# Optimization experiments

Hardware: AMD Instinct MI355X
Metric: run time of the kernel (lower is better)

The kernel has to match this reference:

```python
import jax, jax.numpy as jnp
import numpy as np

B, N, S, C, H = 16, 64, 4096, 768, 8
HD = C // H
SCALE = HD ** -0.5
ASSIGN_EPS = 1.0


def hard_softmax(logits, axis):
    # softmax over `axis`, then straight-through one-hot argmax along `axis`
    y_soft = jax.nn.softmax(logits, axis=axis)
    idx = jnp.argmax(y_soft, axis=axis, keepdims=True)
    n = logits.shape[axis]
    shape = [1] * logits.ndim
    shape[axis] = n
    iota = jnp.arange(n).reshape(shape)
    y_hard = (iota == idx).astype(logits.dtype)
    return y_hard - jax.lax.stop_gradient(y_soft) + y_soft


def setup_inputs() -> dict:
    key = jax.random.key(0)
    ks = jax.random.split(key, 7)
    w = lambda k, shp: (jax.random.normal(k, shp, dtype=jnp.float32) * 0.02)
    return {
        'query': jax.random.normal(ks[0], (B, N, C), dtype=jnp.float32),
        'key_in': jax.random.normal(ks[1], (B, S, C), dtype=jnp.float32),
        'Wq': w(ks[2], (C, C)),
        'Wk': w(ks[3], (C, C)),
        'Wv': w(ks[4], (C, C)),
        'Wo': w(ks[5], (C, C)),
        'bo': jnp.zeros((C,), dtype=jnp.float32),
    }


def reference(query, key_in, Wq, Wk, Wv, Wo, bo):
    # linear projections (torch Linear: x @ W.T), split heads -> b h n d
    q = jnp.einsum('bnc,dc->bnd', query, Wq).reshape(B, N, H, HD).transpose(0, 2, 1, 3)
    k = jnp.einsum('bsc,dc->bsd', key_in, Wk).reshape(B, S, H, HD).transpose(0, 2, 1, 3)
    v = jnp.einsum('bsc,dc->bsd', key_in, Wv).reshape(B, S, H, HD).transpose(0, 2, 1, 3)
    raw_attn = jnp.einsum('bhnd,bhsd->bhns', q, k) * SCALE      # [B,H,N,S]
    attn = hard_softmax(raw_attn, axis=-2)                       # hard assign over groups N
    attn = attn / (attn.sum(axis=-1, keepdims=True) + ASSIGN_EPS)  # renorm over tokens S
    out = jnp.einsum('bhns,bhsd->bhnd', attn, v)                 # [B,H,N,HD]
    out = out.transpose(0, 2, 1, 3).reshape(B, N, C)
    out = jnp.einsum('bnc,dc->bnd', out, Wo) + bo
    return out
```

## Files before the change

kernel.cpp:

```cpp
#include <hip/hip_runtime.h>

#define BB 16
#define NN 64
#define SS 4096
#define CC 768
#define HH 8
#define HD 96

typedef __attribute__((ext_vector_type(8))) short bf16x8;
typedef __attribute__((ext_vector_type(4))) float f32x4;

static __device__ __forceinline__ unsigned short f2bf(float x) {
  unsigned u = __float_as_uint(x);
  unsigned r = (u + 0x7fffu + ((u >> 16) & 1u)) >> 16;
  return (unsigned short)r;
}
static __device__ __forceinline__ float bf2f(unsigned short h) {
  return __uint_as_float(((unsigned)h) << 16);
}
static __device__ __forceinline__ void split2t(float f0, float f1,
                                               unsigned* hw, unsigned* lw) {
  unsigned u0 = __float_as_uint(f0), u1 = __float_as_uint(f1);
  *hw = (u0 >> 16) | (u1 & 0xffff0000u);
  float l0 = f0 - __uint_as_float(u0 & 0xffff0000u);
  float l1 = f1 - __uint_as_float(u1 & 0xffff0000u);
  unsigned v0 = __float_as_uint(l0), v1 = __float_as_uint(l1);
  *lw = (v0 >> 16) | (v1 & 0xffff0000u);
}

__global__ __launch_bounds__(256) void k_transpose(
    const float* __restrict__ src, float* __restrict__ dst) {
  __shared__ float tile[32][33];
  const int bx = blockIdx.x % 24, by = blockIdx.x / 24;
  const int tx = threadIdx.x & 31, ty = threadIdx.x >> 5;
#pragma unroll
  for (int k = 0; k < 4; ++k)
    tile[ty + k * 8][tx] = src[(size_t)(by * 32 + ty + k * 8) * CC + bx * 32 + tx];
  __syncthreads();
#pragma unroll
  for (int k = 0; k < 4; ++k)
    dst[(size_t)(bx * 32 + ty + k * 8) * CC + by * 32 + tx] = tile[tx][ty + k * 8];
}

__global__ __launch_bounds__(256) void k_qkfold(
    const float* __restrict__ query, const float* __restrict__ WqT,
    const float* __restrict__ Wk, double* __restrict__ qk64,
    unsigned short* __restrict__ qhp, unsigned short* __restrict__ qlp) {
  __shared__ double qin[2][CC];
  __shared__ double q64[2][CC];
  const int tid = threadIdx.x;
  const int r0 = blockIdx.x * 2;

#pragma unroll
  for (int u = 0; u < 6; ++u) {
    int idx = tid + u * 256;
    int r = idx / CC, c = idx - r * CC;
    qin[r][c] = (double)query[(size_t)(r0 + r) * CC + c];
  }
  __syncthreads();

  {
    double a00 = 0.0, a01 = 0.0, a02 = 0.0;
    double a10 = 0.0, a11 = 0.0, a12 = 0.0;
    const float* wt = WqT + tid;
    for (int e = 0; e < CC; ++e) {
      const double q0 = qin[0][e], q1 = qin[1][e];
      const float* w = wt + (size_t)e * CC;
      const double w0 = (double)w[0], w1 = (double)w[256], w2 = (double)w[512];
      a00 += q0 * w0; a01 += q0 * w1; a02 += q0 * w2;
      a10 += q1 * w0; a11 += q1 * w1; a12 += q1 * w2;
    }
    q64[0][tid] = a00; q64[0][tid + 256] = a01; q64[0][tid + 512] = a02;
    q64[1][tid] = a10; q64[1][tid + 256] = a11; q64[1][tid + 512] = a12;
  }
  __syncthreads();

  const double SC = 0.10206207261596575;
  for (int h = 0; h < HH; ++h) {
    double b00 = 0.0, b01 = 0.0, b02 = 0.0;
    double b10 = 0.0, b11 = 0.0, b12 = 0.0;
    const float* wk = Wk + (size_t)(h * HD) * CC + tid;
    const double* qh0 = &q64[0][h * HD];
    const double* qh1 = &q64[1][h * HD];
#pragma unroll 4
    for (int dd = 0; dd < HD; ++dd) {
      const float* w = wk + (size_t)dd * CC;
      const double w0 = (double)w[0], w1 = (double)w[256], w2 = (double)w[512];
      const double q0 = qh0[dd], q1 = qh1[dd];
      b00 += q0 * w0; b01 += q0 * w1; b02 += q0 * w2;
      b10 += q1 * w0; b11 += q1 * w1; b12 += q1 * w2;
    }
    double av[2][3] = {{b00 * SC, b01 * SC, b02 * SC},
                       {b10 * SC, b11 * SC, b12 * SC}};
#pragma unroll
    for (int r = 0; r < 2; ++r) {
      const int row = r0 + r, b_ = row >> 6, n = row & 63;
      const int col512 = h * 64 + n;
#pragma unroll
      for (int m = 0; m < 3; ++m) {
        const int c = tid + m * 256;
        size_t o = ((size_t)(b_ * HH + h) * NN + n) * CC + c;
        qk64[o] = av[r][m];
        float f = (float)av[r][m];
        unsigned short hh16 = f2bf(f);
        const int cs = c >> 5, lkc = (c >> 3) & 3, j = c & 7;
        size_t po = (((size_t)(b_ * 24 + cs) * 32 + (col512 >> 4)) * 64 +
                     (lkc * 16 + (col512 & 15))) * 8 + j;
        qhp[po] = hh16;
        qlp[po] = f2bf(f - bf2f(hh16));
      }
    }
  }
}

#define DELTA 1e-3f

__global__ __launch_bounds__(512) void k_filter_mfma(
    const float* __restrict__ key,
    const unsigned short* __restrict__ qhp, const unsigned short* __restrict__ qlp,
    unsigned char* __restrict__ assign_t, int* __restrict__ susp,
    int* __restrict__ scnt) {
  __shared__ float alds[2][64][68];
  const int tid = threadIdx.x;
  const int lane = tid & 63;
  const int wn = tid >> 6;
  const int bid0 = blockIdx.x;
  const int swz = (bid0 & 7) * 128 + (bid0 >> 3);
  const int b = swz >> 6;
  const int s0 = (swz & 63) * 64;
  const int l16 = lane & 15;
  const int lk = lane >> 4;

  f32x4 acc[4][4];
#pragma unroll
  for (int m = 0; m < 4; ++m)
#pragma unroll
    for (int n = 0; n < 4; ++n) acc[m][n] = (f32x4){0.f, 0.f, 0.f, 0.f};

  const float* kbase = key + ((size_t)b * SS + s0) * CC;
  const int srow = tid >> 3, sc8 = tid & 7;

#define BBASE(cs) ((((size_t)(b * 24 + (cs)) * 32 + wn * 4) * 64 + lane) * 8)

  bf16x8 bhA[4], blA[4], bhB[4], blB[4];
  {
    float4 st0 = *(const float4*)(kbase + (size_t)srow * CC + sc8 * 8);
    float4 st1 = *(const float4*)(kbase + (size_t)srow * CC + sc8 * 8 + 4);
    *(float4*)&alds[0][srow][sc8 * 8] = st0;
    *(float4*)&alds[0][srow][sc8 * 8 + 4] = st1;
    const size_t bb = BBASE(0);
#pragma unroll
    for (int n = 0; n < 4; ++n) {
      bhA[n] = *(const bf16x8*)(qhp + bb + (size_t)n * 512);
      blA[n] = *(const bf16x8*)(qlp + bb + (size_t)n * 512);
    }
  }
  __syncthreads();

  for (int t = 0; t < 12; ++t) {
    const int cur = t & 1;
    float4 st0, st1;
    if (t < 11) {
      const int cb = (t + 1) * 64;
      st0 = *(const float4*)(kbase + (size_t)srow * CC + cb + sc8 * 8);
      st1 = *(const float4*)(kbase + (size_t)srow * CC + cb + sc8 * 8 + 4);
    }
    {
      const int cs = t * 2;
      const size_t bbn = BBASE(cs + 1);
#pragma unroll
      for (int n = 0; n < 4; ++n) {
        bhB[n] = *(const bf16x8*)(qhp + bbn + (size_t)n * 512);
        blB[n] = *(const bf16x8*)(qlp + bbn + (size_t)n * 512);
      }
      union { bf16x8 v; unsigned w[4]; } ah[4], al[4];
#pragma unroll
      for (int m = 0; m < 4; ++m) {
        const float* ap = &alds[cur][m * 16 + l16][lk * 8];
        float4 x0 = *(const float4*)ap;
        float4 x1 = *(const float4*)(ap + 4);
        split2t(x0.x, x0.y, &ah[m].w[0], &al[m].w[0]);
        split2t(x0.z, x0.w, &ah[m].w[1], &al[m].w[1]);
        split2t(x1.x, x1.y, &ah[m].w[2], &al[m].w[2]);
        split2t(x1.z, x1.w, &ah[m].w[3], &al[m].w[3]);
      }
#pragma unroll
      for (int m = 0; m < 4; ++m)
#pragma unroll
        for (int n = 0; n < 4; ++n)
          acc[m][n] = __builtin_amdgcn_mfma_f32_16x16x32_bf16(ah[m].v, bhA[n], acc[m][n], 0, 0, 0);
#pragma unroll
      for (int m = 0; m < 4; ++m)
#pragma unroll
        for (int n = 0; n < 4; ++n)
          acc[m][n] = __builtin_amdgcn_mfma_f32_16x16x32_bf16(ah[m].v, blA[n], acc[m][n], 0, 0, 0);
#pragma unroll
      for (int m = 0; m < 4; ++m)
#pragma unroll
        for (int n = 0; n < 4; ++n)
          acc[m][n] = __builtin_amdgcn_mfma_f32_16x16x32_bf16(al[m].v, bhA[n], acc[m][n], 0, 0, 0);
    }
    {
      if (t < 11) {
        const size_t bbn = BBASE(t * 2 + 2);
#pragma unroll
        for (int n = 0; n < 4; ++n) {
          bhA[n] = *(const bf16x8*)(qhp + bbn + (size_t)n * 512);
          blA[n] = *(const bf16x8*)(qlp + bbn + (size_t)n * 512);
        }
      }
      union { bf16x8 v; unsigned w[4]; } ah[4], al[4];
#pragma unroll
      for (int m = 0; m < 4; ++m) {
        const float* ap = &alds[cur][m * 16 + l16][32 + lk * 8];
        float4 x0 = *(const float4*)ap;
        float4 x1 = *(const float4*)(ap + 4);
        split2t(x0.x, x0.y, &ah[m].w[0], &al[m].w[0]);
        split2t(x0.z, x0.w, &ah[m].w[1], &al[m].w[1]);
        split2t(x1.x, x1.y, &ah[m].w[2], &al[m].w[2]);
        split2t(x1.z, x1.w, &ah[m].w[3], &al[m].w[3]);
      }
#pragma unroll
      for (int m = 0; m < 4; ++m)
#pragma unroll
        for (int n = 0; n < 4; ++n)
          acc[m][n] = __builtin_amdgcn_mfma_f32_16x16x32_bf16(ah[m].v, bhB[n], acc[m][n], 0, 0, 0);
#pragma unroll
      for (int m = 0; m < 4; ++m)
#pragma unroll
        for (int n = 0; n < 4; ++n)
          acc[m][n] = __builtin_amdgcn_mfma_f32_16x16x32_bf16(ah[m].v, blB[n], acc[m][n], 0, 0, 0);
#pragma unroll
      for (int m = 0; m < 4; ++m)
#pragma unroll
        for (int n = 0; n < 4; ++n)
          acc[m][n] = __builtin_amdgcn_mfma_f32_16x16x32_bf16(al[m].v, bhB[n], acc[m][n], 0, 0, 0);
    }

    if (t < 11) {
      *(float4*)&alds[cur ^ 1][srow][sc8 * 8] = st0;
      *(float4*)&alds[cur ^ 1][srow][sc8 * 8 + 4] = st1;
    }
    __syncthreads();
  }
#undef BBASE

#pragma unroll
  for (int m = 0; m < 4; ++m) {
    const int tokbase = s0 + m * 16 + lk * 4;
#pragma unroll
    for (int r = 0; r < 4; ++r) {
      const int tok = tokbase + r;
      float m1 = -3.402823466e38f, m2 = -3.402823466e38f;
      int i1 = 0;
#pragma unroll
      for (int n = 0; n < 4; ++n) {
        float v = acc[m][n][r];
        int g = n * 16 + l16;
        if (v > m1) { m2 = m1; m1 = v; i1 = g; }
        else if (v > m2) m2 = v;
      }
#pragma unroll
      for (int off = 1; off <= 8; off <<= 1) {
        float om1 = __shfl_xor(m1, off);
        float om2 = __shfl_xor(m2, off);
        int oi1 = __shfl_xor(i1, off);
        if (om1 > m1 || (om1 == m1 && oi1 < i1)) {
          m2 = fmaxf(m1, fmaxf(m2, om2));
          m1 = om1; i1 = oi1;
        } else {
          m2 = fmaxf(om1, fmaxf(m2, om2));
        }
      }
      if (l16 == 0) {
        const int bh2 = b * 8 + wn;
        assign_t[((size_t)b * SS + tok) * 8 + wn] = (unsigned char)i1;
        if (m1 - m2 < DELTA) {
          int w = atomicAdd(&scnt[bh2], 1);
          susp[(size_t)bh2 * SS + w] = tok;
        }
      }
    }
  }
}

__global__ __launch_bounds__(256) void k_rescore(
    const float* __restrict__ key, const double* __restrict__ qk64,
    const int* __restrict__ susp, const int* __restrict__ scnt,
    unsigned char* __restrict__ assign_t) {
  __shared__ float krow[16][CC];
  __shared__ double l64[16][64];
  const int bh = blockIdx.x;
  const int cnt = scnt[bh];
  if (cnt == 0) return;
  const int b = bh >> 3, h = bh & 7;
  const int tid = threadIdx.x;
  const int n = tid >> 2, q = tid & 3;
  const double* qrow = qk64 + ((size_t)bh * NN + n) * CC + q * 192;

  for (int i0 = 0; i0 < cnt; i0 += 16) {
    const int nb = (cnt - i0 < 16) ? (cnt - i0) : 16;
    for (int r = 0; r < nb; ++r) {
      const int s = susp[(size_t)bh * SS + i0 + r];
      for (int u = tid; u < CC; u += 256)
        krow[r][u] = key[((size_t)b * SS + s) * CC + u];
    }
    __syncthreads();

    double acc[16];
#pragma unroll
    for (int r = 0; r < 16; ++r) acc[r] = 0.0;
    for (int c4 = 0; c4 < 48; ++c4) {
      const double w0 = qrow[c4 * 4 + 0];
      const double w1 = qrow[c4 * 4 + 1];
      const double w2 = qrow[c4 * 4 + 2];
      const double w3 = qrow[c4 * 4 + 3];
#pragma unroll
      for (int r = 0; r < 16; ++r) {
        float4 k4 = *(const float4*)&krow[r][q * 192 + c4 * 4];
        acc[r] += w0 * (double)k4.x;
        acc[r] += w1 * (double)k4.y;
        acc[r] += w2 * (double)k4.z;
        acc[r] += w3 * (double)k4.w;
      }
    }
#pragma unroll
    for (int r = 0; r < 16; ++r) {
      acc[r] += __shfl_xor(acc[r], 1);
      acc[r] += __shfl_xor(acc[r], 2);
    }
    if (q == 0) {
#pragma unroll
      for (int r = 0; r < 16; ++r) l64[r][n] = acc[r];
    }
    __syncthreads();
    if (tid < nb) {
      double best = l64[tid][0];
      int bi = 0;
      for (int n2 = 1; n2 < 64; ++n2)
        if (l64[tid][n2] > best) { best = l64[tid][n2]; bi = n2; }
      const int s = susp[(size_t)bh * SS + i0 + tid];
      assign_t[((size_t)b * SS + s) * 8 + h] = (unsigned char)bi;
    }
    __syncthreads();
  }
}

__global__ __launch_bounds__(256) void k_counts(
    const unsigned char* __restrict__ assign_t, int* __restrict__ counts) {
  __shared__ int hist[64];
  const int bh = blockIdx.x;
  const int b = bh >> 3, h = bh & 7;
  const int tid = threadIdx.x;
  if (tid < 64) hist[tid] = 0;
  __syncthreads();
  for (int s = tid; s < SS; s += 256)
    atomicAdd(&hist[assign_t[((size_t)b * SS + s) * 8 + h]], 1);
  __syncthreads();
  if (tid < 64) counts[bh * 64 + tid] = hist[tid];
}

__global__ __launch_bounds__(64) void k_rank(
    const unsigned char* __restrict__ assign_t, const int* __restrict__ counts,
    int* __restrict__ offsets, int* __restrict__ perm) {
  __shared__ int base[64];
  const int bh = blockIdx.x;
  const int b = bh >> 3, h = bh & 7;
  const int lane = threadIdx.x;

  int cn = counts[bh * 64 + lane];
  int off = cn;
#pragma unroll
  for (int d = 1; d < 64; d <<= 1) {
    int t = __shfl_up(off, d);
    if (lane >= d) off += t;
  }
  off -= cn;
  offsets[bh * 64 + lane] = off;
  base[lane] = off;

  for (int c = 0; c < SS / 64; ++c) {
    const int s = c * 64 + lane;
    const int g = (int)assign_t[((size_t)b * SS + s) * 8 + h];
    unsigned long long m = ~0ull;
#pragma unroll
    for (int k = 0; k < 6; ++k) {
      unsigned long long bk = __ballot((g >> k) & 1);
      m &= ((g >> k) & 1) ? bk : ~bk;
    }
    const int leader = __ffsll((unsigned long long)m) - 1;
    const int rankin = __popcll(m & ((1ull << lane) - 1ull));
    int baseo = 0;
    if (lane == leader) {
      baseo = base[g];
      base[g] = baseo + __popcll(m);
    }
    baseo = __shfl(baseo, leader);
    perm[(size_t)bh * SS + baseo + rankin] = s;
  }
}

__global__ __launch_bounds__(64) void k_gatherp(
    const float* __restrict__ key, const int* __restrict__ perm,
    const int* __restrict__ offsets, const int* __restrict__ counts,
    float* __restrict__ gsum) {
  const int bid = blockIdx.x;
  const int bh = bid >> 6;
  const int b = bh >> 3;
  const int lane = threadIdx.x;

  const int off = offsets[bid];
  const int cnt = counts[bid];
  const int* pl = perm + (size_t)bh * SS + off;
  const float* kb = key + (size_t)b * SS * CC;

  float4 a0 = {0.f, 0.f, 0.f, 0.f}, b0 = a0, c0 = a0;
  int j = 0;
  for (; j + 3 < cnt; j += 4) {
    const int s0 = pl[j], s1 = pl[j + 1], s2 = pl[j + 2], s3 = pl[j + 3];
    const float4* k0 = (const float4*)(kb + (size_t)s0 * CC);
    const float4* k1 = (const float4*)(kb + (size_t)s1 * CC);
    const float4* k2 = (const float4*)(kb + (size_t)s2 * CC);
    const float4* k3 = (const float4*)(kb + (size_t)s3 * CC);
    float4 x0 = k0[lane], x1 = k0[lane + 64], x2 = k0[lane + 128];
    float4 y0 = k1[lane], y1 = k1[lane + 64], y2 = k1[lane + 128];
    float4 z0 = k2[lane], z1 = k2[lane + 64], z2 = k2[lane + 128];
    float4 w0 = k3[lane], w1 = k3[lane + 64], w2 = k3[lane + 128];
    a0.x += x0.x; a0.y += x0.y; a0.z += x0.z; a0.w += x0.w;
    b0.x += x1.x; b0.y += x1.y; b0.z += x1.z; b0.w += x1.w;
    c0.x += x2.x; c0.y += x2.y; c0.z += x2.z; c0.w += x2.w;
    a0.x += y0.x; a0.y += y0.y; a0.z += y0.z; a0.w += y0.w;
    b0.x += y1.x; b0.y += y1.y; b0.z += y1.z; b0.w += y1.w;
    c0.x += y2.x; c0.y += y2.y; c0.z += y2.z; c0.w += y2.w;
    a0.x += z0.x; a0.y += z0.y; a0.z += z0.z; a0.w += z0.w;
    b0.x += z1.x; b0.y += z1.y; b0.z += z1.z; b0.w += z1.w;
    c0.x += z2.x; c0.y += z2.y; c0.z += z2.z; c0.w += z2.w;
    a0.x += w0.x; a0.y += w0.y; a0.z += w0.z; a0.w += w0.w;
    b0.x += w1.x; b0.y += w1.y; b0.z += w1.z; b0.w += w1.w;
    c0.x += w2.x; c0.y += w2.y; c0.z += w2.z; c0.w += w2.w;
  }
  for (; j < cnt; ++j) {
    const int s0 = pl[j];
    const float4* k0 = (const float4*)(kb + (size_t)s0 * CC);
    float4 x0 = k0[lane], x1 = k0[lane + 64], x2 = k0[lane + 128];
    a0.x += x0.x; a0.y += x0.y; a0.z += x0.z; a0.w += x0.w;
    b0.x += x1.x; b0.y += x1.y; b0.z += x1.z; b0.w += x1.w;
    c0.x += x2.x; c0.y += x2.y; c0.z += x2.z; c0.w += x2.w;
  }
  float4* go = (float4*)(gsum + (size_t)bid * CC);
  go[lane] = a0; go[lane + 64] = b0; go[lane + 128] = c0;
}

__global__ __launch_bounds__(256) void k_out(
    const float* __restrict__ gsum, const int* __restrict__ counts,
    const float* __restrict__ WvT, const float* __restrict__ WoT,
    const float* __restrict__ bo, float* __restrict__ out) {
  __shared__ float gs[2][HH][CC];
  __shared__ float vr[2][CC];
  const int tid = threadIdx.x;
  const int r0 = blockIdx.x * 2;

  for (int r = 0; r < 2; ++r) {
    int row = r0 + r, b = row >> 6, n = row & 63;
    for (int h = 0; h < HH; ++h) {
      const float sc = 1.f / (float)(counts[(b * HH + h) * NN + n] + 1);
      const float* src = gsum + ((size_t)(b * HH + h) * NN + n) * CC;
      for (int m = 0; m < 3; ++m)
        gs[r][h][tid + m * 256] = src[tid + m * 256] * sc;
    }
  }
  __syncthreads();

  const int h0 = tid / HD, h1 = (tid + 256) / HD, h2 = (tid + 512) / HD;
  {
    float a00 = 0.f, a01 = 0.f, a02 = 0.f;
    float a10 = 0.f, a11 = 0.f, a12 = 0.f;
    const float* wt = WvT + tid;
    for (int e4 = 0; e4 < CC / 4; ++e4) {
      const int e = e4 * 4;
      float4 g00 = *(const float4*)&gs[0][h0][e];
      float4 g01 = *(const float4*)&gs[0][h1][e];
      float4 g02 = *(const float4*)&gs[0][h2][e];
      float4 g10 = *(const float4*)&gs[1][h0][e];
      float4 g11 = *(const float4*)&gs[1][h1][e];
      float4 g12 = *(const float4*)&gs[1][h2][e];
      const float* w0p = wt + (size_t)e * CC;
      const float* w1p = wt + (size_t)(e + 1) * CC;
      const float* w2p = wt + (size_t)(e + 2) * CC;
      const float* w3p = wt + (size_t)(e + 3) * CC;
      float wa = w0p[0], wb = w0p[256], wc = w0p[512];
      a00 = fmaf(g00.x, wa, a00); a01 = fmaf(g01.x, wb, a01); a02 = fmaf(g02.x, wc, a02);
      a10 = fmaf(g10.x, wa, a10); a11 = fmaf(g11.x, wb, a11); a12 = fmaf(g12.x, wc, a12);
      wa = w1p[0]; wb = w1p[256]; wc = w1p[512];
      a00 = fmaf(g00.y, wa, a00); a01 = fmaf(g01.y, wb, a01); a02 = fmaf(g02.y, wc, a02);
      a10 = fmaf(g10.y, wa, a10); a11 = fmaf(g11.y, wb, a11); a12 = fmaf(g12.y, wc, a12);
      wa = w2p[0]; wb = w2p[256]; wc = w2p[512];
      a00 = fmaf(g00.z, wa, a00); a01 = fmaf(g01.z, wb, a01); a02 = fmaf(g02.z, wc, a02);
      a10 = fmaf(g10.z, wa, a10); a11 = fmaf(g11.z, wb, a11); a12 = fmaf(g12.z, wc, a12);
      wa = w3p[0]; wb = w3p[256]; wc = w3p[512];
      a00 = fmaf(g00.w, wa, a00); a01 = fmaf(g01.w, wb, a01); a02 = fmaf(g02.w, wc, a02);
      a10 = fmaf(g10.w, wa, a10); a11 = fmaf(g11.w, wb, a11); a12 = fmaf(g12.w, wc, a12);
    }
    vr[0][tid] = a00; vr[0][tid + 256] = a01; vr[0][tid + 512] = a02;
    vr[1][tid] = a10; vr[1][tid + 256] = a11; vr[1][tid + 512] = a12;
  }
  __syncthreads();

  {
    float a00 = bo[tid], a01 = bo[tid + 256], a02 = bo[tid + 512];
    float a10 = a00, a11 = a01, a12 = a02;
    const float* wt = WoT + tid;
    for (int e4 = 0; e4 < CC / 4; ++e4) {
      const int e = e4 * 4;
      float4 v0 = *(const float4*)&vr[0][e];
      float4 v1 = *(const float4*)&vr[1][e];
      const float* w0p = wt + (size_t)e * CC;
      const float* w1p = wt + (size_t)(e + 1) * CC;
      const float* w2p = wt + (size_t)(e + 2) * CC;
      const float* w3p = wt + (size_t)(e + 3) * CC;
      float wa = w0p[0], wb = w0p[256], wc = w0p[512];
      a00 = fmaf(v0.x, wa, a00); a01 = fmaf(v0.x, wb, a01); a02 = fmaf(v0.x, wc, a02);
      a10 = fmaf(v1.x, wa, a10); a11 = fmaf(v1.x, wb, a11); a12 = fmaf(v1.x, wc, a12);
      wa = w1p[0]; wb = w1p[256]; wc = w1p[512];
      a00 = fmaf(v0.y, wa, a00); a01 = fmaf(v0.y, wb, a01); a02 = fmaf(v0.y, wc, a02);
      a10 = fmaf(v1.y, wa, a10); a11 = fmaf(v1.y, wb, a11); a12 = fmaf(v1.y, wc, a12);
      wa = w2p[0]; wb = w2p[256]; wc = w2p[512];
      a00 = fmaf(v0.z, wa, a00); a01 = fmaf(v0.z, wb, a01); a02 = fmaf(v0.z, wc, a02);
      a10 = fmaf(v1.z, wa, a10); a11 = fmaf(v1.z, wb, a11); a12 = fmaf(v1.z, wc, a12);
      wa = w3p[0]; wb = w3p[256]; wc = w3p[512];
      a00 = fmaf(v0.w, wa, a00); a01 = fmaf(v0.w, wb, a01); a02 = fmaf(v0.w, wc, a02);
      a10 = fmaf(v1.w, wa, a10); a11 = fmaf(v1.w, wb, a11); a12 = fmaf(v1.w, wc, a12);
    }
    out[(size_t)(r0 + 0) * CC + tid] = a00;
    out[(size_t)(r0 + 0) * CC + tid + 256] = a01;
    out[(size_t)(r0 + 0) * CC + tid + 512] = a02;
    out[(size_t)(r0 + 1) * CC + tid] = a10;
    out[(size_t)(r0 + 1) * CC + tid + 256] = a11;
    out[(size_t)(r0 + 1) * CC + tid + 512] = a12;
  }
}

extern "C" void kernel_launch(void* const* d_in, const int* in_sizes, int n_in,
                              void* d_out, int out_size, void* d_ws, size_t ws_size,
                              hipStream_t stream) {
  const float* query = (const float*)d_in[0];
  const float* key   = (const float*)d_in[1];
  const float* Wq    = (const float*)d_in[2];
  const float* Wk    = (const float*)d_in[3];
  const float* Wv    = (const float*)d_in[4];
  const float* Wo    = (const float*)d_in[5];
  const float* bo    = (const float*)d_in[6];
  float* out = (float*)d_out;

  char* ws = (char*)d_ws;
  double* qk64           = (double*)(ws);
  float* gsum            = (float*)(ws);
  unsigned short* qhp    = (unsigned short*)(ws + 50331648);
  unsigned short* qlp    = (unsigned short*)(ws + 62914560);
  unsigned char* assign_t= (unsigned char*)(ws + 75497472);
  int* susp              = (int*)(ws + 76021760);
  int* scnt              = (int*)(ws + 78118912);
  int* counts            = (int*)(ws + 78119424);
  int* offsets           = (int*)(ws + 78152192);
  int* perm              = (int*)(ws + 78184960);
  float* WqT             = (float*)(ws + 80282112);
  float* WvT             = (float*)(ws + 82641408);
  float* WoT             = (float*)(ws + 85000704);

  hipMemsetAsync(scnt, 0, 512, stream);
  k_transpose<<<576, 256, 0, stream>>>(Wq, WqT);
  k_transpose<<<576, 256, 0, stream>>>(Wv, WvT);
  k_transpose<<<576, 256, 0, stream>>>(Wo, WoT);
  k_qkfold<<<512, 256, 0, stream>>>(query, WqT, Wk, qk64, qhp, qlp);
  k_filter_mfma<<<1024, 512, 0, stream>>>(key, qhp, qlp, assign_t, susp, scnt);
  k_rescore<<<128, 256, 0, stream>>>(key, qk64, susp, scnt, assign_t);
  k_counts<<<128, 256, 0, stream>>>(assign_t, counts);
  k_rank<<<128, 64, 0, stream>>>(assign_t, counts, offsets, perm);
  k_gatherp<<<8192, 64, 0, stream>>>(key, perm, offsets, counts, gsum);
  k_out<<<512, 256, 0, stream>>>(gsum, counts, WvT, WoT, bo, out);
}
```

Measured before the change: 883.8 us.

## Pre-convert key to bf16 in half-batch chunks before gather-sum

Adds a conversion kernel that turns one half of the batch's key tensor into bf16 in workspace. The gather-sum then reads bf16 rows instead of fp32, split into two passes of eight batches each so the converted buffer stays small. The goal is to halve the bytes each head's gather pulls from memory, since every key row is read once per head. In exchange it adds an extra full read and half-size write of the key tensor, and it introduces bf16 rounding into the group sums, which could hurt accuracy against the fp32 reference.

```diff
diff --git a/kernel.cpp b/kernel.cpp
--- a/kernel.cpp
+++ b/kernel.cpp
@@ -9,6 +9,7 @@
 
 typedef __attribute__((ext_vector_type(8))) short bf16x8;
 typedef __attribute__((ext_vector_type(4))) float f32x4;
+typedef __attribute__((ext_vector_type(8))) unsigned short u16x8;
 
 static __device__ __forceinline__ unsigned short f2bf(float x) {
   unsigned u = __float_as_uint(x);
@@ -360,6 +361,21 @@
   if (tid < 64) counts[bh * 64 + tid] = hist[tid];
 }
 
+__global__ __launch_bounds__(256) void k_convert(
+    const float* __restrict__ keyhalf, unsigned short* __restrict__ kb16) {
+  const int n8 = 8 * SS * CC / 8;
+  int i = blockIdx.x * 256 + threadIdx.x;
+  const int stride = gridDim.x * 256;
+  for (; i < n8; i += stride) {
+    float4 a = ((const float4*)keyhalf)[i * 2];
+    float4 b = ((const float4*)keyhalf)[i * 2 + 1];
+    u16x8 r;
+    r[0] = f2bf(a.x); r[1] = f2bf(a.y); r[2] = f2bf(a.z); r[3] = f2bf(a.w);
+    r[4] = f2bf(b.x); r[5] = f2bf(b.y); r[6] = f2bf(b.z); r[7] = f2bf(b.w);
+    *(u16x8*)(kb16 + (size_t)i * 8) = r;
+  }
+}
+
 __global__ __launch_bounds__(64) void k_rank(
     const unsigned char* __restrict__ assign_t, const int* __restrict__ counts,
     int* __restrict__ offsets, int* __restrict__ perm) {
@@ -401,54 +417,55 @@
 }
 
 __global__ __launch_bounds__(64) void k_gatherp(
-    const float* __restrict__ key, const int* __restrict__ perm,
+    const unsigned short* __restrict__ kb16, const int* __restrict__ perm,
     const int* __restrict__ offsets, const int* __restrict__ counts,
-    float* __restrict__ gsum) {
+    float* __restrict__ gsum, int b0) {
   const int bid = blockIdx.x;
-  const int bh = bid >> 6;
-  const int b = bh >> 3;
+  const int bl = bid >> 9;
+  const int gbid = b0 * 512 + bid;
+  const int bh = gbid >> 6;
   const int lane = threadIdx.x;
 
-  const int off = offsets[bid];
-  const int cnt = counts[bid];
+  const int off = offsets[gbid];
+  const int cnt = counts[gbid];
   const int* pl = perm + (size_t)bh * SS + off;
-  const float* kb = key + (size_t)b * SS * CC;
-
-  float4 a0 = {0.f, 0.f, 0.f, 0.f}, b0 = a0, c0 = a0;
+  const unsigned short* kb = kb16 + (size_t)bl * SS * CC;
+
+  float4 a0 = {0.f, 0.f, 0.f, 0.f}, b0v = a0, c0 = a0;
   int j = 0;
   for (; j + 3 < cnt; j += 4) {
     const int s0 = pl[j], s1 = pl[j + 1], s2 = pl[j + 2], s3 = pl[j + 3];
-    const float4* k0 = (const float4*)(kb + (size_t)s0 * CC);
-    const float4* k1 = (const float4*)(kb + (size_t)s1 * CC);
-    const float4* k2 = (const float4*)(kb + (size_t)s2 * CC);
-    const float4* k3 = (const float4*)(kb + (size_t)s3 * CC);
-    float4 x0 = k0[lane], x1 = k0[lane + 64], x2 = k0[lane + 128];
-    float4 y0 = k1[lane], y1 = k1[lane + 64], y2 = k1[lane + 128];
-    float4 z0 = k2[lane], z1 = k2[lane + 64], z2 = k2[lane + 128];
-    float4 w0 = k3[lane], w1 = k3[lane + 64], w2 = k3[lane + 128];
-    a0.x += x0.x; a0.y += x0.y; a0.z += x0.z; a0.w += x0.w;
-    b0.x += x1.x; b0.y += x1.y; b0.z += x1.z; b0.w += x1.w;
-    c0.x += x2.x; c0.y += x2.y; c0.z += x2.z; c0.w += x2.w;
-    a0.x += y0.x; a0.y += y0.y; a0.z += y0.z; a0.w += y0.w;
-    b0.x += y1.x; b0.y += y1.y; b0.z += y1.z; b0.w += y1.w;
-    c0.x += y2.x; c0.y += y2.y; c0.z += y2.z; c0.w += y2.w;
-    a0.x += z0.x; a0.y += z0.y; a0.z += z0.z; a0.w += z0.w;
-    b0.x += z1.x; b0.y += z1.y; b0.z += z1.z; b0.w += z1.w;
-    c0.x += z2.x; c0.y += z2.y; c0.z += z2.z; c0.w += z2.w;
-    a0.x += w0.x; a0.y += w0.y; a0.z += w0.z; a0.w += w0.w;
-    b0.x += w1.x; b0.y += w1.y; b0.z += w1.z; b0.w += w1.w;
-    c0.x += w2.x; c0.y += w2.y; c0.z += w2.z; c0.w += w2.w;
+    const ushort4* k0 = (const ushort4*)(kb + (size_t)s0 * CC);
+    const ushort4* k1 = (const ushort4*)(kb + (size_t)s1 * CC);
+    const ushort4* k2 = (const ushort4*)(kb + (size_t)s2 * CC);
+    const ushort4* k3 = (const ushort4*)(kb + (size_t)s3 * CC);
+    ushort4 x0 = k0[lane], x1 = k0[lane + 64], x2 = k0[lane + 128];
+    ushort4 y0 = k1[lane], y1 = k1[lane + 64], y2 = k1[lane + 128];
+    ushort4 z0 = k2[lane], z1 = k2[lane + 64], z2 = k2[lane + 128];
+    ushort4 w0 = k3[lane], w1 = k3[lane + 64], w2 = k3[lane + 128];
+    a0.x += bf2f(x0.x); a0.y += bf2f(x0.y); a0.z += bf2f(x0.z); a0.w += bf2f(x0.w);
+    b0v.x += bf2f(x1.x); b0v.y += bf2f(x1.y); b0v.z += bf2f(x1.z); b0v.w += bf2f(x1.w);
+    c0.x += bf2f(x2.x); c0.y += bf2f(x2.y); c0.z += bf2f(x2.z); c0.w += bf2f(x2.w);
+    a0.x += bf2f(y0.x); a0.y += bf2f(y0.y); a0.z += bf2f(y0.z); a0.w += bf2f(y0.w);
+    b0v.x += bf2f(y1.x); b0v.y += bf2f(y1.y); b0v.z += bf2f(y1.z); b0v.w += bf2f(y1.w);
+    c0.x += bf2f(y2.x); c0.y += bf2f(y2.y); c0.z += bf2f(y2.z); c0.w += bf2f(y2.w);
+    a0.x += bf2f(z0.x); a0.y += bf2f(z0.y); a0.z += bf2f(z0.z); a0.w += bf2f(z0.w);
+    b0v.x += bf2f(z1.x); b0v.y += bf2f(z1.y); b0v.z += bf2f(z1.z); b0v.w += bf2f(z1.w);
+    c0.x += bf2f(z2.x); c0.y += bf2f(z2.y); c0.z += bf2f(z2.z); c0.w += bf2f(z2.w);
+    a0.x += bf2f(w0.x); a0.y += bf2f(w0.y); a0.z += bf2f(w0.z); a0.w += bf2f(w0.w);
+    b0v.x += bf2f(w1.x); b0v.y += bf2f(w1.y); b0v.z += bf2f(w1.z); b0v.w += bf2f(w1.w);
+    c0.x += bf2f(w2.x); c0.y += bf2f(w2.y); c0.z += bf2f(w2.z); c0.w += bf2f(w2.w);
   }
   for (; j < cnt; ++j) {
     const int s0 = pl[j];
-    const float4* k0 = (const float4*)(kb + (size_t)s0 * CC);
-    float4 x0 = k0[lane], x1 = k0[lane + 64], x2 = k0[lane + 128];
-    a0.x += x0.x; a0.y += x0.y; a0.z += x0.z; a0.w += x0.w;
-    b0.x += x1.x; b0.y += x1.y; b0.z += x1.z; b0.w += x1.w;
-    c0.x += x2.x; c0.y += x2.y; c0.z += x2.z; c0.w += x2.w;
-  }
-  float4* go = (float4*)(gsum + (size_t)bid * CC);
-  go[lane] = a0; go[lane + 64] = b0; go[lane + 128] = c0;
+    const ushort4* k0 = (const ushort4*)(kb + (size_t)s0 * CC);
+    ushort4 x0 = k0[lane], x1 = k0[lane + 64], x2 = k0[lane + 128];
+    a0.x += bf2f(x0.x); a0.y += bf2f(x0.y); a0.z += bf2f(x0.z); a0.w += bf2f(x0.w);
+    b0v.x += bf2f(x1.x); b0v.y += bf2f(x1.y); b0v.z += bf2f(x1.z); b0v.w += bf2f(x1.w);
+    c0.x += bf2f(x2.x); c0.y += bf2f(x2.y); c0.z += bf2f(x2.z); c0.w += bf2f(x2.w);
+  }
+  float4* go = (float4*)(gsum + (size_t)gbid * CC);
+  go[lane] = a0; go[lane + 64] = b0v; go[lane + 128] = c0;
 }
 
 __global__ __launch_bounds__(256) void k_out(
@@ -554,9 +571,10 @@
 
   char* ws = (char*)d_ws;
   double* qk64           = (double*)(ws);
-  float* gsum            = (float*)(ws);
+  unsigned short* kb16   = (unsigned short*)(ws);
   unsigned short* qhp    = (unsigned short*)(ws + 50331648);
   unsigned short* qlp    = (unsigned short*)(ws + 62914560);
+  float* gsum            = (float*)(ws + 50331648);
   unsigned char* assign_t= (unsigned char*)(ws + 75497472);
   int* susp              = (int*)(ws + 76021760);
   int* scnt              = (int*)(ws + 78118912);
@@ -576,6 +594,9 @@
   k_rescore<<<128, 256, 0, stream>>>(key, qk64, susp, scnt, assign_t);
   k_counts<<<128, 256, 0, stream>>>(assign_t, counts);
   k_rank<<<128, 64, 0, stream>>>(assign_t, counts, offsets, perm);
-  k_gatherp<<<8192, 64, 0, stream>>>(key, perm, offsets, counts, gsum);
+  k_convert<<<1024, 256, 0, stream>>>(key, kb16);
+  k_gatherp<<<4096, 64, 0, stream>>>(kb16, perm, offsets, counts, gsum, 0);
+  k_convert<<<1024, 256, 0, stream>>>(key + (size_t)8 * SS * CC, kb16);
+  k_gatherp<<<4096, 64, 0, stream>>>(kb16, perm, offsets, counts, gsum, 8);
   k_out<<<512, 256, 0, stream>>>(gsum, counts, WvT, WoT, bo, out);
 }
```

New measurement: 831.4 us. 1.06x faster.
